# Performance work log

Measured on AMD Instinct MI355X. Metric: run time of the kernel, lower is better.

## Reference

```python
import jax, jax.numpy as jnp
import numpy as np
from math import sqrt

SEQ, NIN, NH, NOUT, HEADS = 4096, 1024, 128, 1024, 8
DOUT = HEADS * (2 * NH + NOUT)  # 10240
EPS = 1e-5

def setup_inputs() -> dict:
    key = jax.random.key(0)
    k1, k2, k3 = jax.random.split(key, 3)
    x = jax.random.normal(k1, (SEQ, NIN), dtype=jnp.float32)
    W = jax.random.normal(k2, (DOUT, NIN), dtype=jnp.float32) * (1.0 / sqrt(NIN))
    b = jax.random.normal(k3, (DOUT,), dtype=jnp.float32) * 0.01
    ln_w = jnp.ones((NOUT,), dtype=jnp.float32)
    ln_b = jnp.zeros((NOUT,), dtype=jnp.float32)
    return {"x": x, "W": W, "b": b, "ln_w": ln_w, "ln_b": ln_b}

def reference(x, W, b, ln_w, ln_b):
    # fused QKV projection: (S, NIN) -> (S, HEADS, 2*NH + NOUT)
    out = (x @ W.T + b).reshape(x.shape[0], HEADS, -1)
    keys, queries, values = jnp.split(out, (NH, 2 * NH), axis=-1)
    keys = keys / sqrt(keys.shape[-1])
    # logits[i, j, h] = sum_k keys[i,h,k] * queries[j,h,k]
    logits = jnp.einsum('ihk,jhk->ijh', keys, queries)
    attention = jax.nn.softmax(logits, axis=1)
    # sum over j and heads -> (S, NOUT)
    output = jnp.einsum('ijh,jhe->ie', attention, values)
    # LayerNorm over last dim, elementwise affine, eps=1e-5
    mean = jnp.mean(output, axis=-1, keepdims=True)
    var = jnp.var(output, axis=-1, keepdims=True)
    normed = (output - mean) / jnp.sqrt(var + EPS)
    return normed * ln_w + ln_b
```

## Files before the change

kernel.cpp:

```cpp
#include <hip/hip_runtime.h>

typedef __attribute__((ext_vector_type(8))) __bf16 bf16x8;
typedef __attribute__((ext_vector_type(4))) __bf16 bf16x4;
typedef __attribute__((ext_vector_type(4))) float f32x4;
typedef __attribute__((ext_vector_type(16))) float f32x16;

#define SEQ   4096
#define NIN   1024
#define DH    128
#define NOUTD 1024
#define HEADS 8
#define CPH   1280
#define L2E   1.44269504f

static __device__ inline f32x16 zero16() {
  f32x16 z;
#pragma unroll
  for (int r = 0; r < 16; ++r) z[r] = 0.f;
  return z;
}

static __device__ inline unsigned pk2(float a, float b) {
  unsigned short ua = __builtin_bit_cast(unsigned short, (__bf16)a);
  unsigned short ub = __builtin_bit_cast(unsigned short, (__bf16)b);
  return (unsigned)ua | ((unsigned)ub << 16);
}

__global__ __launch_bounds__(256) void k_cvt(const float* __restrict__ src,
                                             __bf16* __restrict__ dst, int n) {
  int i = (blockIdx.x * 256 + threadIdx.x) * 4;
  if (i >= n) return;
  float4 v = *(const float4*)(src + i);
  bf16x4 o = { (__bf16)v.x, (__bf16)v.y, (__bf16)v.z, (__bf16)v.w };
  *(bf16x4*)(dst + i) = o;
}

__global__ __launch_bounds__(256) void k_zero(float4* __restrict__ p) {
  p[(size_t)blockIdx.x * 256 + threadIdx.x] = float4{0.f, 0.f, 0.f, 0.f};
}

__global__ __launch_bounds__(256) void k_gemm_qkv(
    const __bf16* __restrict__ xb, const __bf16* __restrict__ wb,
    const float* __restrict__ bias,
    __bf16* __restrict__ Kx, __bf16* __restrict__ Qx, __bf16* __restrict__ Vt)
{
  __shared__ __align__(16) __bf16 As[128 * 32];
  __shared__ __align__(16) __bf16 Bs[128 * 32];
  const int tid = threadIdx.x;
  const int w = tid >> 6, l = tid & 63;
  const int i0 = blockIdx.x * 128;
  const int n0 = blockIdx.y * 128;
  const int lrow = l & 15;
  const int lkb  = (l >> 4) * 16;
  const int soff = (w * 2) * 1024 + l * 16;

  f32x4 acc[4][4] = {};

  for (int kt = 0; kt < 32; ++kt) {
    __syncthreads();
#pragma unroll
    for (int q = 0; q < 2; ++q) {
      int off = soff + q * 1024;
      int row = off >> 6, kb = off & 63;
      const __bf16* ga = xb + (size_t)(i0 + row) * NIN + kt * 32 + (kb >> 1);
      const __bf16* gb = wb + (size_t)(n0 + row) * NIN + kt * 32 + (kb >> 1);
      __builtin_amdgcn_global_load_lds(
          (const __attribute__((address_space(1))) void*)ga,
          (__attribute__((address_space(3))) void*)((char*)As + (w * 2 + q) * 1024),
          16, 0, 0);
      __builtin_amdgcn_global_load_lds(
          (const __attribute__((address_space(1))) void*)gb,
          (__attribute__((address_space(3))) void*)((char*)Bs + (w * 2 + q) * 1024),
          16, 0, 0);
    }
    __syncthreads();
    bf16x8 af[4], bfr[4];
#pragma unroll
    for (int mi = 0; mi < 4; ++mi)
      af[mi] = *(const bf16x8*)((const char*)As + (((w >> 1) * 64 + mi * 16 + lrow) * 64) + lkb);
#pragma unroll
    for (int ni = 0; ni < 4; ++ni)
      bfr[ni] = *(const bf16x8*)((const char*)Bs + (((w & 1) * 64 + ni * 16 + lrow) * 64) + lkb);
#pragma unroll
    for (int mi = 0; mi < 4; ++mi)
#pragma unroll
      for (int ni = 0; ni < 4; ++ni)
        acc[mi][ni] = __builtin_amdgcn_mfma_f32_16x16x32_bf16(af[mi], bfr[ni], acc[mi][ni], 0, 0, 0);
  }

  const int iw = i0 + (w >> 1) * 64;
  const int nw = n0 + (w & 1) * 64;
  const int lhi = l >> 4;
#pragma unroll
  for (int ni = 0; ni < 4; ++ni) {
    int n = nw + ni * 16 + lrow;
    float bv = bias[n];
    int h = n / CPH;
    int c = n - h * CPH;
    if (c < 256) {
#pragma unroll
      for (int mi = 0; mi < 4; ++mi)
#pragma unroll
        for (int r = 0; r < 4; ++r) {
          int i = iw + mi * 16 + lhi * 4 + r;
          float v = acc[mi][ni][r] + bv;
          if (c < 128)
            Kx[(((size_t)h * SEQ + i) << 7) + c] = (__bf16)(v * 0.08838834764831845f);
          else
            Qx[(((size_t)h * SEQ + i) << 7) + (c - 128)] = (__bf16)v;
        }
    } else {
      int e = c - 256;
#pragma unroll
      for (int mi = 0; mi < 4; ++mi) {
        int ib = iw + mi * 16 + lhi * 4;
        bf16x4 pk = { (__bf16)(acc[mi][ni][0] + bv), (__bf16)(acc[mi][ni][1] + bv),
                      (__bf16)(acc[mi][ni][2] + bv), (__bf16)(acc[mi][ni][3] + bv) };
        *(bf16x4*)(Vt + (((size_t)h * NOUTD + e) << 12) + ib) = pk;
      }
    }
  }
}

static __device__ inline void stage_q(const __bf16* Qh, char* dst, int j0,
                                      int tid, int nthr) {
#pragma unroll
  for (int s = tid; s < 1024; s += nthr) {
    int row = s >> 4, ch = s & 15;
    const char* src = (const char*)Qh + (((size_t)(j0 + row)) << 8) +
                      ((ch << 4) ^ ((row & 15) << 4));
    __builtin_amdgcn_global_load_lds(
        (const __attribute__((address_space(1))) void*)src,
        (__attribute__((address_space(3))) void*)(dst + (s << 4)), 16, 0, 0);
  }
}

static __device__ inline void stage_v(const char* Vhb, char* dst, int j0,
                                      int tid) {
#pragma unroll
  for (int s = tid; s < 2048; s += 512) {
    int row = s >> 3, ch = s & 7;
    const char* src = Vhb + ((size_t)row << 13) + ((size_t)j0 << 1) +
                      ((ch << 4) ^ ((row & 7) << 4));
    __builtin_amdgcn_global_load_lds(
        (const __attribute__((address_space(1))) void*)src,
        (__attribute__((address_space(3))) void*)(dst + (s << 4)), 16, 0, 0);
  }
}

__global__ __launch_bounds__(256) void k_stats(
    const __bf16* __restrict__ Kx, const __bf16* __restrict__ Qx,
    float* __restrict__ stat_m, float* __restrict__ stat_il)
{
  __shared__ __align__(16) char Qb[2][16384];
  const int tid = threadIdx.x;
  const int w = tid >> 6, l = tid & 63;
  const int l31 = l & 31, hl = l >> 5;
  const int b = blockIdx.x;
  const int h = b >> 5;
  const int i_base = (b & 31) * 128;
  const __bf16* Kh = Kx + ((size_t)h * SEQ << 7);
  const __bf16* Qh = Qx + ((size_t)h * SEQ << 7);

  bf16x8 kf[8];
#pragma unroll
  for (int c = 0; c < 8; ++c)
    kf[c] = *(const bf16x8*)(Kh + (((size_t)(i_base + 32 * w + l31)) << 7) + c * 16 + hl * 8);

  float m_run = -1e30f, l_run = 0.f;

  stage_q(Qh, Qb[0], 0, tid, 256);
  __syncthreads();

  for (int jt = 0; jt < 64; ++jt) {
    const int cur = jt & 1;
    if (jt < 63) stage_q(Qh, Qb[cur ^ 1], (jt + 1) * 64, tid, 256);
    const char* qb = Qb[cur];

    f32x16 s0 = zero16(), s1 = zero16();
#pragma unroll
    for (int c = 0; c < 8; ++c) {
      int cb = ((2 * c + hl) << 4);
      bf16x8 a0 = *(const bf16x8*)(qb + (l31 << 8) + (cb ^ ((l31 & 15) << 4)));
      bf16x8 a1 = *(const bf16x8*)(qb + ((32 + l31) << 8) + (cb ^ ((l31 & 15) << 4)));
      s0 = __builtin_amdgcn_mfma_f32_32x32x16_bf16(a0, kf[c], s0, 0, 0, 0);
      s1 = __builtin_amdgcn_mfma_f32_32x32x16_bf16(a1, kf[c], s1, 0, 0, 0);
    }

    float pm = -1e30f;
#pragma unroll
    for (int r = 0; r < 16; ++r) pm = fmaxf(pm, fmaxf(s0[r], s1[r]));
    float mn = fmaxf(m_run, pm);
    l_run *= exp2f((m_run - mn) * L2E);
    float a = 0.f;
#pragma unroll
    for (int r = 0; r < 16; ++r)
      a += exp2f((s0[r] - mn) * L2E) + exp2f((s1[r] - mn) * L2E);
    l_run += a;
    m_run = mn;
    __syncthreads();
  }

  float mp = __shfl_xor(m_run, 32);
  float lp = __shfl_xor(l_run, 32);
  float mf = fmaxf(m_run, mp);
  float lf = l_run * exp2f((m_run - mf) * L2E) + lp * exp2f((mp - mf) * L2E);
  if (hl == 0) {
    int i = i_base + 32 * w + l31;
    stat_m[h * SEQ + i] = mf;
    stat_il[h * SEQ + i] = 1.0f / lf;
  }
}

__global__ __launch_bounds__(512, 2) void k_attn2(
    const __bf16* __restrict__ Kx, const __bf16* __restrict__ Qx,
    const __bf16* __restrict__ Vt, const float* __restrict__ stat_m,
    const float* __restrict__ stat_il, float* __restrict__ out)
{
  __shared__ __align__(16) char Qb[2][16384];
  __shared__ __align__(16) char Vb[2][32768];
  __shared__ float s_linv[256];

  const int tid = threadIdx.x;
  const int w = tid >> 6, l = tid & 63;
  const int l31 = l & 31, hl = l >> 5;

  const int b = blockIdx.x;
  const int gLow = b & 7, inner = b >> 3;
  const int g = (inner >> 4) * 8 + gLow;
  const int it = inner & 15;
  const int h = g >> 2, et = g & 3;
  const int i_base = it * 256, e_base = et * 256;

  const __bf16* Kh = Kx + ((size_t)h * SEQ << 7);
  const __bf16* Qh = Qx + ((size_t)h * SEQ << 7);
  const char* Vhb = (const char*)Vt + (((size_t)(h * NOUTD + e_base)) << 13);

  if (tid < 256) s_linv[tid] = stat_il[h * SEQ + i_base + tid];
  const float m_i = stat_m[h * SEQ + i_base + 32 * w + l31];

  bf16x8 kf[8];
#pragma unroll
  for (int c = 0; c < 8; ++c)
    kf[c] = *(const bf16x8*)(Kh + (((size_t)(i_base + 32 * w + l31)) << 7) + c * 16 + hl * 8);

  f32x16 acc[8];
#pragma unroll
  for (int n = 0; n < 8; ++n) acc[n] = zero16();

  stage_q(Qh, Qb[0], 0, tid, 512);
  stage_v(Vhb, Vb[0], 0, tid);
  __syncthreads();

  for (int jt = 0; jt < 64; ++jt) {
    const int cur = jt & 1;
    const int j0n = (jt + 1) * 64;
    if (jt < 63) {
      stage_q(Qh, Qb[cur ^ 1], j0n, tid, 512);
      stage_v(Vhb, Vb[cur ^ 1], j0n, tid);
    }
    const char* qb = Qb[cur];
    const char* vb = Vb[cur];

    f32x16 s0 = zero16(), s1 = zero16();
#pragma unroll
    for (int c = 0; c < 8; ++c) {
      int cb = ((2 * c + hl) << 4);
      bf16x8 a0 = *(const bf16x8*)(qb + (l31 << 8) + (cb ^ ((l31 & 15) << 4)));
      bf16x8 a1 = *(const bf16x8*)(qb + ((32 + l31) << 8) + (cb ^ ((l31 & 15) << 4)));
      s0 = __builtin_amdgcn_mfma_f32_32x32x16_bf16(a0, kf[c], s0, 0, 0, 0);
      s1 = __builtin_amdgcn_mfma_f32_32x32x16_bf16(a1, kf[c], s1, 0, 0, 0);
    }

    bf16x8 pf[4];
#pragma unroll
    for (int c2 = 0; c2 < 4; ++c2) {
      const f32x16& sv = (c2 >> 1) ? s1 : s0;
      const int base = (c2 & 1) * 8;
      float e0 = exp2f((sv[base + 0] - m_i) * L2E);
      float e1 = exp2f((sv[base + 1] - m_i) * L2E);
      float e2 = exp2f((sv[base + 2] - m_i) * L2E);
      float e3 = exp2f((sv[base + 3] - m_i) * L2E);
      float e4 = exp2f((sv[base + 4] - m_i) * L2E);
      float e5 = exp2f((sv[base + 5] - m_i) * L2E);
      float e6 = exp2f((sv[base + 6] - m_i) * L2E);
      float e7 = exp2f((sv[base + 7] - m_i) * L2E);
      unsigned WA0 = pk2(e0, e1), WA1 = pk2(e2, e3);
      unsigned WB0 = pk2(e4, e5), WB1 = pk2(e6, e7);
      unsigned send0 = hl ? WA0 : WB0;
      unsigned send1 = hl ? WA1 : WB1;
      unsigned r0 = (unsigned)__shfl_xor((int)send0, 32);
      unsigned r1 = (unsigned)__shfl_xor((int)send1, 32);
      int4 qd;
      qd.x = (int)(hl ? r0 : WA0);
      qd.y = (int)(hl ? r1 : WA1);
      qd.z = (int)(hl ? WB0 : r0);
      qd.w = (int)(hl ? WB1 : r1);
      pf[c2] = __builtin_bit_cast(bf16x8, qd);
    }

#pragma unroll
    for (int n = 0; n < 8; ++n) {
      const int erow = 32 * n + l31;
      const char* vrow = vb + (erow << 7);
      const int sw = (erow & 7) << 4;
#pragma unroll
      for (int c2 = 0; c2 < 4; ++c2) {
        bf16x8 bv = *(const bf16x8*)(vrow + ((((2 * c2 + hl) << 4)) ^ sw));
        acc[n] = __builtin_amdgcn_mfma_f32_32x32x16_bf16(pf[c2], bv, acc[n], 0, 0, 0);
      }
    }
    __syncthreads();
  }

#pragma unroll
  for (int n = 0; n < 8; ++n) {
    const int e = e_base + 32 * n + l31;
#pragma unroll
    for (int r = 0; r < 16; ++r) {
      int iloc = 32 * w + (r & 3) + 8 * (r >> 2) + 4 * hl;
      float v = acc[n][r] * s_linv[iloc];
      atomicAdd(out + (((size_t)(i_base + iloc)) << 10) + e, v);
    }
  }
}

__global__ __launch_bounds__(256) void k_ln(float* __restrict__ io,
                                            const float* __restrict__ lw,
                                            const float* __restrict__ lb) {
  const int i = blockIdx.x, t = threadIdx.x;
  const int w = t >> 6, l = t & 63;
  float4 v = *(const float4*)(io + ((size_t)i << 10) + t * 4);
  float s = v.x + v.y + v.z + v.w;
  float q = v.x * v.x + v.y * v.y + v.z * v.z + v.w * v.w;
#pragma unroll
  for (int d = 1; d < 64; d <<= 1) {
    s += __shfl_xor(s, d);
    q += __shfl_xor(q, d);
  }
  __shared__ float red[4][2];
  if (l == 0) { red[w][0] = s; red[w][1] = q; }
  __syncthreads();
  s = red[0][0] + red[1][0] + red[2][0] + red[3][0];
  q = red[0][1] + red[1][1] + red[2][1] + red[3][1];
  float mean = s * (1.0f / 1024.0f);
  float var = q * (1.0f / 1024.0f) - mean * mean;
  float rstd = rsqrtf(var + 1e-5f);
  float4 gw = *(const float4*)(lw + t * 4);
  float4 gb = *(const float4*)(lb + t * 4);
  float4 ov;
  ov.x = (v.x - mean) * rstd * gw.x + gb.x;
  ov.y = (v.y - mean) * rstd * gw.y + gb.y;
  ov.z = (v.z - mean) * rstd * gw.z + gb.z;
  ov.w = (v.w - mean) * rstd * gw.w + gb.w;
  *(float4*)(io + ((size_t)i << 10) + t * 4) = ov;
}

extern "C" void kernel_launch(void* const* d_in, const int* in_sizes, int n_in,
                              void* d_out, int out_size, void* d_ws, size_t ws_size,
                              hipStream_t stream) {
  (void)in_sizes; (void)n_in; (void)out_size; (void)ws_size;
  const float* x  = (const float*)d_in[0];
  const float* W  = (const float*)d_in[1];
  const float* b  = (const float*)d_in[2];
  const float* lw = (const float*)d_in[3];
  const float* lb = (const float*)d_in[4];
  float* out = (float*)d_out;
  char* ws = (char*)d_ws;

  __bf16* xb = (__bf16*)ws;
  __bf16* wb = (__bf16*)(ws + (size_t)8  * 1024 * 1024);
  __bf16* Kx = (__bf16*)(ws + (size_t)28 * 1024 * 1024);
  __bf16* Qx = (__bf16*)(ws + (size_t)36 * 1024 * 1024);
  __bf16* Vt = (__bf16*)(ws + (size_t)44 * 1024 * 1024);
  float* stat_m  = (float*)ws;
  float* stat_il = (float*)(ws + (size_t)128 * 1024);

  k_cvt<<<4096, 256, 0, stream>>>(x, xb, SEQ * NIN);
  k_cvt<<<10240, 256, 0, stream>>>(W, wb, HEADS * CPH * NIN);
  k_gemm_qkv<<<dim3(32, 80), 256, 0, stream>>>(xb, wb, b, Kx, Qx, Vt);
  k_zero<<<4096, 256, 0, stream>>>((float4*)out);
  k_stats<<<256, 256, 0, stream>>>(Kx, Qx, stat_m, stat_il);
  k_attn2<<<512, 512, 0, stream>>>(Kx, Qx, Vt, stat_m, stat_il, out);
  k_ln<<<4096, 256, 0, stream>>>(out, lw, lb);
}
```

Measured before the change: 831.3 us.

## Relayout Q and V into MFMA-fragment order and retile attention waves

```diff
diff --git a/kernel.cpp b/kernel.cpp
--- a/kernel.cpp
+++ b/kernel.cpp
@@ -42,7 +42,7 @@
 __global__ __launch_bounds__(256) void k_gemm_qkv(
     const __bf16* __restrict__ xb, const __bf16* __restrict__ wb,
     const float* __restrict__ bias,
-    __bf16* __restrict__ Kx, __bf16* __restrict__ Qx, __bf16* __restrict__ Vt)
+    __bf16* __restrict__ Kx, __bf16* __restrict__ Q2, __bf16* __restrict__ V2)
 {
   __shared__ __align__(16) __bf16 As[128 * 32];
   __shared__ __align__(16) __bf16 Bs[128 * 32];
@@ -97,59 +97,42 @@
     float bv = bias[n];
     int h = n / CPH;
     int c = n - h * CPH;
-    if (c < 256) {
+    if (c < 128) {
 #pragma unroll
       for (int mi = 0; mi < 4; ++mi)
 #pragma unroll
         for (int r = 0; r < 4; ++r) {
           int i = iw + mi * 16 + lhi * 4 + r;
           float v = acc[mi][ni][r] + bv;
-          if (c < 128)
-            Kx[(((size_t)h * SEQ + i) << 7) + c] = (__bf16)(v * 0.08838834764831845f);
-          else
-            Qx[(((size_t)h * SEQ + i) << 7) + (c - 128)] = (__bf16)v;
+          Kx[(((size_t)h * SEQ + i) << 7) + c] = (__bf16)(v * 0.08838834764831845f);
+        }
+    } else if (c < 256) {
+      int d = c - 128;
+      size_t qEl = ((size_t)(h * 16 + (d >> 3)) << 15) + (size_t)(d & 7);
+#pragma unroll
+      for (int mi = 0; mi < 4; ++mi)
+#pragma unroll
+        for (int r = 0; r < 4; ++r) {
+          int j = iw + mi * 16 + lhi * 4 + r;
+          Q2[qEl + ((size_t)j << 3)] = (__bf16)(acc[mi][ni][r] + bv);
         }
     } else {
       int e = c - 256;
 #pragma unroll
       for (int mi = 0; mi < 4; ++mi) {
-        int ib = iw + mi * 16 + lhi * 4;
+        int jb = iw + mi * 16 + lhi * 4;
+        int J = jb >> 3, js = jb & 7;
+        size_t vEl = (((size_t)(h * 512 + J)) << 13) + ((size_t)e << 3) + js;
         bf16x4 pk = { (__bf16)(acc[mi][ni][0] + bv), (__bf16)(acc[mi][ni][1] + bv),
                       (__bf16)(acc[mi][ni][2] + bv), (__bf16)(acc[mi][ni][3] + bv) };
-        *(bf16x4*)(Vt + (((size_t)h * NOUTD + e) << 12) + ib) = pk;
-      }
-    }
-  }
-}
-
-static __device__ inline void stage_q(const __bf16* Qh, char* dst, int j0,
-                                      int tid, int nthr) {
-#pragma unroll
-  for (int s = tid; s < 1024; s += nthr) {
-    int row = s >> 4, ch = s & 15;
-    const char* src = (const char*)Qh + (((size_t)(j0 + row)) << 8) +
-                      ((ch << 4) ^ ((row & 15) << 4));
-    __builtin_amdgcn_global_load_lds(
-        (const __attribute__((address_space(1))) void*)src,
-        (__attribute__((address_space(3))) void*)(dst + (s << 4)), 16, 0, 0);
-  }
-}
-
-static __device__ inline void stage_v(const char* Vhb, char* dst, int j0,
-                                      int tid) {
-#pragma unroll
-  for (int s = tid; s < 2048; s += 512) {
-    int row = s >> 3, ch = s & 7;
-    const char* src = Vhb + ((size_t)row << 13) + ((size_t)j0 << 1) +
-                      ((ch << 4) ^ ((row & 7) << 4));
-    __builtin_amdgcn_global_load_lds(
-        (const __attribute__((address_space(1))) void*)src,
-        (__attribute__((address_space(3))) void*)(dst + (s << 4)), 16, 0, 0);
+        *(bf16x4*)(V2 + vEl) = pk;
+      }
+    }
   }
 }
 
 __global__ __launch_bounds__(256) void k_stats(
-    const __bf16* __restrict__ Kx, const __bf16* __restrict__ Qx,
+    const __bf16* __restrict__ Kx, const __bf16* __restrict__ Q2,
     float* __restrict__ stat_m, float* __restrict__ stat_il)
 {
   __shared__ __align__(16) char Qb[2][16384];
@@ -160,7 +143,7 @@
   const int h = b >> 5;
   const int i_base = (b & 31) * 128;
   const __bf16* Kh = Kx + ((size_t)h * SEQ << 7);
-  const __bf16* Qh = Qx + ((size_t)h * SEQ << 7);
+  const char* q2b = (const char*)Q2 + ((size_t)h << 20);
 
   bf16x8 kf[8];
 #pragma unroll
@@ -169,20 +152,36 @@
 
   float m_run = -1e30f, l_run = 0.f;
 
-  stage_q(Qh, Qb[0], 0, tid, 256);
+#pragma unroll
+  for (int k = 0; k < 4; ++k) {
+    int s = tid + k * 256;
+    const char* src = q2b + ((size_t)(s >> 6) << 16) + (size_t)(s & 63) * 16;
+    __builtin_amdgcn_global_load_lds(
+        (const __attribute__((address_space(1))) void*)src,
+        (__attribute__((address_space(3))) void*)(Qb[0] + s * 16), 16, 0, 0);
+  }
   __syncthreads();
 
   for (int jt = 0; jt < 64; ++jt) {
     const int cur = jt & 1;
-    if (jt < 63) stage_q(Qh, Qb[cur ^ 1], (jt + 1) * 64, tid, 256);
+    if (jt < 63) {
+      int j0n = (jt + 1) * 64;
+#pragma unroll
+      for (int k = 0; k < 4; ++k) {
+        int s = tid + k * 256;
+        const char* src = q2b + ((size_t)(s >> 6) << 16) + (size_t)(j0n + (s & 63)) * 16;
+        __builtin_amdgcn_global_load_lds(
+            (const __attribute__((address_space(1))) void*)src,
+            (__attribute__((address_space(3))) void*)(Qb[cur ^ 1] + s * 16), 16, 0, 0);
+      }
+    }
     const char* qb = Qb[cur];
 
     f32x16 s0 = zero16(), s1 = zero16();
 #pragma unroll
     for (int c = 0; c < 8; ++c) {
-      int cb = ((2 * c + hl) << 4);
-      bf16x8 a0 = *(const bf16x8*)(qb + (l31 << 8) + (cb ^ ((l31 & 15) << 4)));
-      bf16x8 a1 = *(const bf16x8*)(qb + ((32 + l31) << 8) + (cb ^ ((l31 & 15) << 4)));
+      bf16x8 a0 = *(const bf16x8*)(qb + (((2 * c + hl) * 64 + l31) << 4));
+      bf16x8 a1 = *(const bf16x8*)(qb + (((2 * c + hl) * 64 + 32 + l31) << 4));
       s0 = __builtin_amdgcn_mfma_f32_32x32x16_bf16(a0, kf[c], s0, 0, 0, 0);
       s1 = __builtin_amdgcn_mfma_f32_32x32x16_bf16(a1, kf[c], s1, 0, 0, 0);
     }
@@ -212,52 +211,80 @@
   }
 }
 
-__global__ __launch_bounds__(512, 2) void k_attn2(
-    const __bf16* __restrict__ Kx, const __bf16* __restrict__ Qx,
-    const __bf16* __restrict__ Vt, const float* __restrict__ stat_m,
+__global__ __launch_bounds__(512, 2) void k_attn3(
+    const __bf16* __restrict__ Kx, const __bf16* __restrict__ Q2,
+    const __bf16* __restrict__ V2, const float* __restrict__ stat_m,
     const float* __restrict__ stat_il, float* __restrict__ out)
 {
-  __shared__ __align__(16) char Qb[2][16384];
-  __shared__ __align__(16) char Vb[2][32768];
+  __shared__ __align__(16) char Qb[2][8192];
+  __shared__ __align__(16) char Vb[2][16384];
   __shared__ float s_linv[256];
 
   const int tid = threadIdx.x;
   const int w = tid >> 6, l = tid & 63;
   const int l31 = l & 31, hl = l >> 5;
+  const int islot = w & 3, eslot = w >> 2;
 
   const int b = blockIdx.x;
-  const int gLow = b & 7, inner = b >> 3;
-  const int g = (inner >> 4) * 8 + gLow;
-  const int it = inner & 15;
-  const int h = g >> 2, et = g & 3;
+  const int et = b & 3;
+  const int h = ((b >> 2) & 1) + 2 * (b >> 7);
+  const int it = (b >> 3) & 15;
   const int i_base = it * 256, e_base = et * 256;
 
   const __bf16* Kh = Kx + ((size_t)h * SEQ << 7);
-  const __bf16* Qh = Qx + ((size_t)h * SEQ << 7);
-  const char* Vhb = (const char*)Vt + (((size_t)(h * NOUTD + e_base)) << 13);
+  const char* q2b = (const char*)Q2 + ((size_t)h << 20);
+  const char* v2b = (const char*)V2 + ((size_t)(h * 512) << 14) + ((size_t)e_base << 4);
 
   if (tid < 256) s_linv[tid] = stat_il[h * SEQ + i_base + tid];
-  const float m_i = stat_m[h * SEQ + i_base + 32 * w + l31];
-
-  bf16x8 kf[8];
-#pragma unroll
-  for (int c = 0; c < 8; ++c)
-    kf[c] = *(const bf16x8*)(Kh + (((size_t)(i_base + 32 * w + l31)) << 7) + c * 16 + hl * 8);
-
-  f32x16 acc[8];
-#pragma unroll
-  for (int n = 0; n < 8; ++n) acc[n] = zero16();
-
-  stage_q(Qh, Qb[0], 0, tid, 512);
-  stage_v(Vhb, Vb[0], 0, tid);
+  const int iw0 = i_base + islot * 64;
+  const float m0 = stat_m[h * SEQ + iw0 + l31];
+  const float m1 = stat_m[h * SEQ + iw0 + 32 + l31];
+
+  bf16x8 kf[2][8];
+#pragma unroll
+  for (int ig = 0; ig < 2; ++ig)
+#pragma unroll
+    for (int c = 0; c < 8; ++c)
+      kf[ig][c] = *(const bf16x8*)(Kh + (((size_t)(iw0 + ig * 32 + l31)) << 7) + c * 16 + hl * 8);
+
+  f32x16 acc[2][4];
+#pragma unroll
+  for (int ig = 0; ig < 2; ++ig)
+#pragma unroll
+    for (int n = 0; n < 4; ++n) acc[ig][n] = zero16();
+
+  {
+    const char* srcQ = q2b + ((size_t)(tid >> 5) << 16) + (size_t)(tid & 31) * 16;
+    __builtin_amdgcn_global_load_lds(
+        (const __attribute__((address_space(1))) void*)srcQ,
+        (__attribute__((address_space(3))) void*)(Qb[0] + tid * 16), 16, 0, 0);
+#pragma unroll
+    for (int k = 0; k < 2; ++k) {
+      int s = tid + k * 512;
+      const char* srcV = v2b + ((size_t)(s >> 8) << 14) + (size_t)(s & 255) * 16;
+      __builtin_amdgcn_global_load_lds(
+          (const __attribute__((address_space(1))) void*)srcV,
+          (__attribute__((address_space(3))) void*)(Vb[0] + s * 16), 16, 0, 0);
+    }
+  }
   __syncthreads();
 
-  for (int jt = 0; jt < 64; ++jt) {
+  for (int jt = 0; jt < 128; ++jt) {
     const int cur = jt & 1;
-    const int j0n = (jt + 1) * 64;
-    if (jt < 63) {
-      stage_q(Qh, Qb[cur ^ 1], j0n, tid, 512);
-      stage_v(Vhb, Vb[cur ^ 1], j0n, tid);
+    if (jt < 127) {
+      const int j0n = (jt + 1) * 32;
+      const char* srcQ = q2b + ((size_t)(tid >> 5) << 16) + (size_t)(j0n + (tid & 31)) * 16;
+      __builtin_amdgcn_global_load_lds(
+          (const __attribute__((address_space(1))) void*)srcQ,
+          (__attribute__((address_space(3))) void*)(Qb[cur ^ 1] + tid * 16), 16, 0, 0);
+#pragma unroll
+      for (int k = 0; k < 2; ++k) {
+        int s = tid + k * 512;
+        const char* srcV = v2b + ((size_t)((jt + 1) * 4 + (s >> 8)) << 14) + (size_t)(s & 255) * 16;
+        __builtin_amdgcn_global_load_lds(
+            (const __attribute__((address_space(1))) void*)srcV,
+            (__attribute__((address_space(3))) void*)(Vb[cur ^ 1] + s * 16), 16, 0, 0);
+      }
     }
     const char* qb = Qb[cur];
     const char* vb = Vb[cur];
@@ -265,64 +292,66 @@
     f32x16 s0 = zero16(), s1 = zero16();
 #pragma unroll
     for (int c = 0; c < 8; ++c) {
-      int cb = ((2 * c + hl) << 4);
-      bf16x8 a0 = *(const bf16x8*)(qb + (l31 << 8) + (cb ^ ((l31 & 15) << 4)));
-      bf16x8 a1 = *(const bf16x8*)(qb + ((32 + l31) << 8) + (cb ^ ((l31 & 15) << 4)));
-      s0 = __builtin_amdgcn_mfma_f32_32x32x16_bf16(a0, kf[c], s0, 0, 0, 0);
-      s1 = __builtin_amdgcn_mfma_f32_32x32x16_bf16(a1, kf[c], s1, 0, 0, 0);
-    }
-
-    bf16x8 pf[4];
-#pragma unroll
-    for (int c2 = 0; c2 < 4; ++c2) {
-      const f32x16& sv = (c2 >> 1) ? s1 : s0;
-      const int base = (c2 & 1) * 8;
-      float e0 = exp2f((sv[base + 0] - m_i) * L2E);
-      float e1 = exp2f((sv[base + 1] - m_i) * L2E);
-      float e2 = exp2f((sv[base + 2] - m_i) * L2E);
-      float e3 = exp2f((sv[base + 3] - m_i) * L2E);
-      float e4 = exp2f((sv[base + 4] - m_i) * L2E);
-      float e5 = exp2f((sv[base + 5] - m_i) * L2E);
-      float e6 = exp2f((sv[base + 6] - m_i) * L2E);
-      float e7 = exp2f((sv[base + 7] - m_i) * L2E);
-      unsigned WA0 = pk2(e0, e1), WA1 = pk2(e2, e3);
-      unsigned WB0 = pk2(e4, e5), WB1 = pk2(e6, e7);
-      unsigned send0 = hl ? WA0 : WB0;
-      unsigned send1 = hl ? WA1 : WB1;
-      unsigned r0 = (unsigned)__shfl_xor((int)send0, 32);
-      unsigned r1 = (unsigned)__shfl_xor((int)send1, 32);
-      int4 qd;
-      qd.x = (int)(hl ? r0 : WA0);
-      qd.y = (int)(hl ? r1 : WA1);
-      qd.z = (int)(hl ? WB0 : r0);
-      qd.w = (int)(hl ? WB1 : r1);
-      pf[c2] = __builtin_bit_cast(bf16x8, qd);
-    }
-
-#pragma unroll
-    for (int n = 0; n < 8; ++n) {
-      const int erow = 32 * n + l31;
-      const char* vrow = vb + (erow << 7);
-      const int sw = (erow & 7) << 4;
-#pragma unroll
-      for (int c2 = 0; c2 < 4; ++c2) {
-        bf16x8 bv = *(const bf16x8*)(vrow + ((((2 * c2 + hl) << 4)) ^ sw));
-        acc[n] = __builtin_amdgcn_mfma_f32_32x32x16_bf16(pf[c2], bv, acc[n], 0, 0, 0);
-      }
-    }
+      bf16x8 a0 = *(const bf16x8*)(qb + (((2 * c + hl) * 32 + l31) << 4));
+      s0 = __builtin_amdgcn_mfma_f32_32x32x16_bf16(a0, kf[0][c], s0, 0, 0, 0);
+      s1 = __builtin_amdgcn_mfma_f32_32x32x16_bf16(a0, kf[1][c], s1, 0, 0, 0);
+    }
+
+    bf16x8 pf[2][2];
+#pragma unroll
+    for (int ig = 0; ig < 2; ++ig) {
+      const f32x16& sv = ig ? s1 : s0;
+      const float mi = ig ? m1 : m0;
+#pragma unroll
+      for (int c2 = 0; c2 < 2; ++c2) {
+        const int base = 8 * c2;
+        float e0 = exp2f((sv[base + 0] - mi) * L2E);
+        float e1 = exp2f((sv[base + 1] - mi) * L2E);
+        float e2 = exp2f((sv[base + 2] - mi) * L2E);
+        float e3 = exp2f((sv[base + 3] - mi) * L2E);
+        float e4 = exp2f((sv[base + 4] - mi) * L2E);
+        float e5 = exp2f((sv[base + 5] - mi) * L2E);
+        float e6 = exp2f((sv[base + 6] - mi) * L2E);
+        float e7 = exp2f((sv[base + 7] - mi) * L2E);
+        unsigned WA0 = pk2(e0, e1), WA1 = pk2(e2, e3);
+        unsigned WB0 = pk2(e4, e5), WB1 = pk2(e6, e7);
+        unsigned send0 = hl ? WA0 : WB0;
+        unsigned send1 = hl ? WA1 : WB1;
+        unsigned r0 = (unsigned)__shfl_xor((int)send0, 32);
+        unsigned r1 = (unsigned)__shfl_xor((int)send1, 32);
+        int4 qd;
+        qd.x = (int)(hl ? r0 : WA0);
+        qd.y = (int)(hl ? r1 : WA1);
+        qd.z = (int)(hl ? WB0 : r0);
+        qd.w = (int)(hl ? WB1 : r1);
+        pf[ig][c2] = __builtin_bit_cast(bf16x8, qd);
+      }
+    }
+
+#pragma unroll
+    for (int c2 = 0; c2 < 2; ++c2)
+#pragma unroll
+      for (int n = 0; n < 4; ++n) {
+        bf16x8 bv = *(const bf16x8*)(vb + (((2 * c2 + hl) * 256 + eslot * 128 + 32 * n + l31) << 4));
+        acc[0][n] = __builtin_amdgcn_mfma_f32_32x32x16_bf16(pf[0][c2], bv, acc[0][n], 0, 0, 0);
+        acc[1][n] = __builtin_amdgcn_mfma_f32_32x32x16_bf16(pf[1][c2], bv, acc[1][n], 0, 0, 0);
+      }
     __syncthreads();
   }
 
 #pragma unroll
-  for (int n = 0; n < 8; ++n) {
-    const int e = e_base + 32 * n + l31;
-#pragma unroll
-    for (int r = 0; r < 16; ++r) {
-      int iloc = 32 * w + (r & 3) + 8 * (r >> 2) + 4 * hl;
-      float v = acc[n][r] * s_linv[iloc];
-      atomicAdd(out + (((size_t)(i_base + iloc)) << 10) + e, v);
-    }
-  }
+  for (int ig = 0; ig < 2; ++ig)
+#pragma unroll
+    for (int n = 0; n < 4; ++n) {
+      const int e = e_base + eslot * 128 + 32 * n + l31;
+#pragma unroll
+      for (int r = 0; r < 16; ++r) {
+        int row = (r & 3) + 8 * (r >> 2) + 4 * hl;
+        int iloc = islot * 64 + ig * 32 + row;
+        float v = acc[ig][n][r] * s_linv[iloc];
+        atomicAdd(out + (((size_t)(i_base + iloc)) << 10) + e, v);
+      }
+    }
 }
 
 __global__ __launch_bounds__(256) void k_ln(float* __restrict__ io,
@@ -371,16 +400,16 @@
   __bf16* xb = (__bf16*)ws;
   __bf16* wb = (__bf16*)(ws + (size_t)8  * 1024 * 1024);
   __bf16* Kx = (__bf16*)(ws + (size_t)28 * 1024 * 1024);
-  __bf16* Qx = (__bf16*)(ws + (size_t)36 * 1024 * 1024);
-  __bf16* Vt = (__bf16*)(ws + (size_t)44 * 1024 * 1024);
+  __bf16* Q2 = (__bf16*)(ws + (size_t)36 * 1024 * 1024);
+  __bf16* V2 = (__bf16*)(ws + (size_t)44 * 1024 * 1024);
   float* stat_m  = (float*)ws;
   float* stat_il = (float*)(ws + (size_t)128 * 1024);
 
   k_cvt<<<4096, 256, 0, stream>>>(x, xb, SEQ * NIN);
   k_cvt<<<10240, 256, 0, stream>>>(W, wb, HEADS * CPH * NIN);
-  k_gemm_qkv<<<dim3(32, 80), 256, 0, stream>>>(xb, wb, b, Kx, Qx, Vt);
+  k_gemm_qkv<<<dim3(32, 80), 256, 0, stream>>>(xb, wb, b, Kx, Q2, V2);
   k_zero<<<4096, 256, 0, stream>>>((float4*)out);
-  k_stats<<<256, 256, 0, stream>>>(Kx, Qx, stat_m, stat_il);
-  k_attn2<<<512, 512, 0, stream>>>(Kx, Qx, Vt, stat_m, stat_il, out);
+  k_stats<<<256, 256, 0, stream>>>(Kx, Q2, stat_m, stat_il);
+  k_attn3<<<512, 512, 0, stream>>>(Kx, Q2, V2, stat_m, stat_il, out);
   k_ln<<<4096, 256, 0, stream>>>(out, lw, lb);
 }
```

New measurement: 1.011 ms. 1.22x slower.
